# Performance work log

Measured on AMD Instinct MI355X. Metric: run time of the kernel, lower is better.

## Reference

```python
import math
import jax, jax.numpy as jnp
import numpy as np

IMG = 512; P = 16; CIN = 3; COUT = 3; E = 768; NHEADS = 12; L = 8
NPH = IMG // P            # 32 patches per side
N = NPH * NPH             # 1024 tokens (must match learned 1024x1024 attn bias)
HD = E // NHEADS          # 64
INTER = min(E // 2, 128)  # 128, OutputProjection intermediate
EPS = 1e-5


def _sin_pe(n_h, n_w, d):
    # faithful port of get_2d_sinusoidal_encoding (second half stays zero)
    pe = np.zeros((n_h, n_w, d), dtype=np.float32)
    dq, dh = d // 4, d // 2
    div = np.exp(np.arange(0, dq, 2, dtype=np.float32) * (-math.log(10000.0) / dq))
    pr = np.arange(n_h, dtype=np.float32)[:, None]
    pc = np.arange(n_w, dtype=np.float32)[:, None]
    pe[:, :, 0:dq:2] = np.sin(pr * div)[:, None, :]
    pe[:, :, 1:dq:2] = np.cos(pr * div)[:, None, :]
    pe[:, :, dq:dh:2] = np.sin(pc * div)[None, :, :]
    pe[:, :, dq + 1:dh:2] = np.cos(pc * div)[None, :, :]
    return jnp.asarray(pe.reshape(-1, d))


def _ln(x, g, b):
    m = x.mean(-1, keepdims=True)
    v = ((x - m) ** 2).mean(-1, keepdims=True)
    return (x - m) * jax.lax.rsqrt(v + EPS) * g + b


def setup_inputs():
    key = jax.random.key(0)
    ks = iter(jax.random.split(key, 32))
    def nrm(shape, scale=0.02):
        return jax.random.normal(next(ks), shape, jnp.float32) * scale
    return {
        'x': jax.random.normal(next(ks), (2, CIN, IMG, IMG), jnp.float32),
        'conv_w': nrm((E, CIN, P, P)), 'conv_b': jnp.zeros((E,), jnp.float32),
        'ln1_g': jnp.ones((L, E), jnp.float32), 'ln1_b': jnp.zeros((L, E), jnp.float32),
        'qkv_w': nrm((L, 3 * E, E)),
        'proj_w': nrm((L, E, E)), 'proj_b': jnp.zeros((L, E), jnp.float32),
        'attn_bias': jax.random.normal(next(ks), (L, N, N), jnp.float32),  # torch.randn init
        'ln2_g': jnp.ones((L, E), jnp.float32), 'ln2_b': jnp.zeros((L, E), jnp.float32),
        'mlp_w1': nrm((L, 2 * E, E)), 'mlp_b1': jnp.zeros((L, 2 * E), jnp.float32),
        'mlp_w2': nrm((L, E, 2 * E)), 'mlp_b2': jnp.zeros((L, E), jnp.float32),
        'op_w1': nrm((INTER, E)), 'op_b1': jnp.zeros((INTER,), jnp.float32),
        'op_w2': nrm((P * P * COUT, INTER)), 'op_b2': jnp.zeros((P * P * COUT,), jnp.float32),
        'ag_wg': nrm((1, COUT), 0.2), 'ag_bng_w': jnp.ones((), jnp.float32), 'ag_bng_b': jnp.zeros((), jnp.float32),
        'ag_wx': nrm((1, CIN), 0.2), 'ag_bnx_w': jnp.ones((), jnp.float32), 'ag_bnx_b': jnp.zeros((), jnp.float32),
        'ag_psi_w': jnp.full((), 0.5, jnp.float32), 'ag_psi_b': jnp.zeros((), jnp.float32),
    }


def reference(x, conv_w, conv_b, ln1_g, ln1_b, qkv_w, proj_w, proj_b, attn_bias,
              ln2_g, ln2_b, mlp_w1, mlp_b1, mlp_w2, mlp_b2,
              op_w1, op_b1, op_w2, op_b2,
              ag_wg, ag_bng_w, ag_bng_b, ag_wx, ag_bnx_w, ag_bnx_b, ag_psi_w, ag_psi_b):
    B = x.shape[0]
    # --- VisionTransformerInput: patch-embed conv (stride == kernel) as reshape+GEMM ---
    xp = x.reshape(B, CIN, NPH, P, NPH, P).transpose(0, 2, 4, 1, 3, 5).reshape(B, N, CIN * P * P)
    t = xp @ conv_w.reshape(E, -1).T + conv_b
    t = t + _sin_pe(NPH, NPH, E)[None]

    # --- encoder blocks (scan over stacked per-layer params) ---
    def block(t, p):
        y = _ln(t, p['ln1_g'], p['ln1_b'])
        qkv = (y @ p['qkv_w'].T).reshape(B, N, 3, NHEADS, HD).transpose(2, 0, 3, 1, 4)
        q, k, v = qkv[0], qkv[1], qkv[2]
        s = jnp.einsum('bhnd,bhmd->bhnm', q, k) / math.sqrt(HD)
        # NOTE: relative_position_bias is computed but never added in the source (dead code);
        # only the learned (N,N) bias parameter is added.
        s = s + p['attn_bias'][None, None]
        a = jax.nn.softmax(s, axis=-1)
        o = jnp.einsum('bhnm,bhmd->bhnd', a, v).transpose(0, 2, 1, 3).reshape(B, N, E)
        o = o @ p['proj_w'].T + p['proj_b']
        t = t + (y + o)  # MHA has an extra internal residual (out = x + out) in the source
        h = _ln(t, p['ln2_g'], p['ln2_b'])
        h = jax.nn.gelu(h @ p['mlp_w1'].T + p['mlp_b1'], approximate=False) @ p['mlp_w2'].T + p['mlp_b2']
        return t + h, None

    stacked = {'ln1_g': ln1_g, 'ln1_b': ln1_b, 'qkv_w': qkv_w, 'proj_w': proj_w,
               'proj_b': proj_b, 'attn_bias': attn_bias, 'ln2_g': ln2_g, 'ln2_b': ln2_b,
               'mlp_w1': mlp_w1, 'mlp_b1': mlp_b1, 'mlp_w2': mlp_w2, 'mlp_b2': mlp_b2}
    t, _ = jax.lax.scan(block, t, stacked)

    # --- OutputProjection: MLP -> Fold -> attention gate -> (identity) interpolate ---
    h = jax.nn.relu(t @ op_w1.T + op_b1) @ op_w2.T + op_b2  # (B, N, C*P*P)
    # nn.Fold(kernel=stride=P): columns interpreted as (C, P, P)
    g = h.reshape(B, NPH, NPH, COUT, P, P).transpose(0, 3, 1, 4, 2, 5).reshape(B, COUT, IMG, IMG)
    inv = 1.0 / math.sqrt(1.0 + EPS)  # BatchNorm eval: running_mean=0, running_var=1
    g1 = jnp.einsum('bchw,oc->bohw', g, ag_wg) * (inv * ag_bng_w) + ag_bng_b
    x1 = jnp.einsum('bchw,oc->bohw', x, ag_wx) * (inv * ag_bnx_w) + ag_bnx_b
    psi = jax.nn.sigmoid(jax.nn.relu(g1 + x1) * ag_psi_w + ag_psi_b)
    out = g * (x * psi)  # x * att_gate's psi == skip_gated; then x_fold * skip_gated
    # F.interpolate to (output_size, output_size) with output_size == image_size: identity
    return out
```

## Files before the change

kernel.cpp:

```cpp
#include <hip/hip_runtime.h>
#include <math.h>

typedef unsigned short u16;
typedef unsigned int u32;
typedef __attribute__((ext_vector_type(8))) short bf16x8;
typedef __attribute__((ext_vector_type(16))) float f32x16;
typedef __attribute__((ext_vector_type(4))) float f4v;
typedef __attribute__((ext_vector_type(4))) u32 u32x4;

#define MFMA(a, b, c) __builtin_amdgcn_mfma_f32_32x32x16_bf16(a, b, c, 0, 0, 0)

#define SYNC_STEP() do {                                   \
    asm volatile("s_waitcnt vmcnt(0)" ::: "memory");       \
    __builtin_amdgcn_s_barrier();                          \
    __builtin_amdgcn_sched_barrier(0);                     \
} while (0)

#define SYNC_CNT_LIT(nlit) do {                                    \
    asm volatile("s_waitcnt vmcnt(" #nlit ")" ::: "memory");       \
    __builtin_amdgcn_s_barrier();                                  \
    __builtin_amdgcn_sched_barrier(0);                             \
} while (0)

__device__ __forceinline__ float bf2f(u16 h) { return __uint_as_float(((u32)h) << 16); }

__device__ __forceinline__ void split2(float v, u16& h, u16& l) {
    u32 u = __float_as_uint(v);
    u32 hr = (u + 0x7FFFu + ((u >> 16) & 1u)) & 0xFFFF0000u;
    h = (u16)(hr >> 16);
    float lf = v - __uint_as_float(hr);
    u32 ul = __float_as_uint(lf);
    l = (u16)((ul + 0x7FFFu + ((ul >> 16) & 1u)) >> 16);
}

__device__ __forceinline__ u32 cvtpk(float lo, float hi) {
    u32 r;
    asm("v_cvt_pk_bf16_f32 %0, %1, %2" : "=v"(r) : "v"(lo), "v"(hi));
    return r;
}

__device__ __forceinline__ void swap32(u32& a, u32& b, int hi) {
    u32 ta = (u32)__shfl_xor((int)a, 32);
    u32 tb = (u32)__shfl_xor((int)b, 32);
    u32 na = hi ? tb : a;
    u32 nb = hi ? b : ta;
    a = na; b = nb;
}

__device__ __forceinline__ void repack(const f32x16& v, int base, int hi, bf16x8& fh, bf16x8& fl) {
    float p0 = v[base + 0], p1 = v[base + 1], p2 = v[base + 2], p3 = v[base + 3];
    float p4 = v[base + 4], p5 = v[base + 5], p6 = v[base + 6], p7 = v[base + 7];
    u32 X0 = cvtpk(p0, p1), X1 = cvtpk(p2, p3), X4 = cvtpk(p4, p5), X5 = cvtpk(p6, p7);
    float r0 = p0 - __uint_as_float(X0 << 16);
    float r1 = p1 - __uint_as_float(X0 & 0xFFFF0000u);
    float r2 = p2 - __uint_as_float(X1 << 16);
    float r3 = p3 - __uint_as_float(X1 & 0xFFFF0000u);
    float r4 = p4 - __uint_as_float(X4 << 16);
    float r5 = p5 - __uint_as_float(X4 & 0xFFFF0000u);
    float r6 = p6 - __uint_as_float(X5 << 16);
    float r7 = p7 - __uint_as_float(X5 & 0xFFFF0000u);
    u32 L0 = cvtpk(r0, r1), L1 = cvtpk(r2, r3), L4 = cvtpk(r4, r5), L5 = cvtpk(r6, r7);
    swap32(X0, X4, hi); swap32(X1, X5, hi);
    swap32(L0, L4, hi); swap32(L1, L5, hi);
    u32x4 th = {X0, X1, X4, X5};
    u32x4 tl = {L0, L1, L4, L5};
    fh = __builtin_bit_cast(bf16x8, th);
    fl = __builtin_bit_cast(bf16x8, tl);
}

__global__ __launch_bounds__(256) void pe_kernel(float* __restrict__ pe) {
    int idx = blockIdx.x * 256 + threadIdx.x;
    int n = idx / 768, d = idx - n * 768;
    float v = 0.0f;
    if (d < 384) {
        int pos = (d < 192) ? (n >> 5) : (n & 31);
        int dd  = (d < 192) ? d : d - 192;
        int j2  = dd & ~1;
        float dv  = expf((float)j2 * (-9.210340371976184f / 192.0f));
        float ang = (float)pos * dv;
        v = (dd & 1) ? cosf(ang) : sinf(ang);
    }
    pe[idx] = v;
}

__global__ __launch_bounds__(256) void gather_kernel(const float* __restrict__ x,
                                                     u16* __restrict__ xph,
                                                     u16* __restrict__ xpl) {
    int idx = blockIdx.x * 256 + threadIdx.x;
    int m = idx / 768, col = idx - m * 768;
    int b = m >> 10, n = m & 1023;
    int ci = col >> 8, rem = col & 255;
    int pr = rem >> 4, pc = rem & 15;
    int hh = ((n >> 5) << 4) + pr;
    int ww = ((n & 31) << 4) + pc;
    float v = x[(((size_t)(b * 3 + ci) * 512) + hh) * 512 + ww];
    split2(v, xph[idx], xpl[idx]);
}

__global__ __launch_bounds__(256) void fsplit(const float* __restrict__ in,
                                              u16* __restrict__ h, u16* __restrict__ l, int n4) {
    int i = blockIdx.x * 256 + threadIdx.x;
    if (i >= n4) return;
    float4 v = ((const float4*)in)[i];
    int o = i * 4;
    split2(v.x, h[o], l[o]);
    split2(v.y, h[o + 1], l[o + 1]);
    split2(v.z, h[o + 2], l[o + 2]);
    split2(v.w, h[o + 3], l[o + 3]);
}

__global__ __launch_bounds__(256) void wsplit_layer(const float* __restrict__ qkvw,
                                                    const float* __restrict__ projw,
                                                    const float* __restrict__ w1,
                                                    const float* __restrict__ w2,
                                                    u16* __restrict__ wh, u16* __restrict__ wl) {
    int i4 = blockIdx.x * 256 + threadIdx.x;
    if (i4 >= 1179648) return;
    size_t idx = (size_t)i4 * 4;
    const float* src; size_t off;
    if (idx < 1769472)      { src = qkvw;  off = idx; }
    else if (idx < 2359296) { src = projw; off = idx - 1769472; }
    else if (idx < 3538944) { src = w1;    off = idx - 2359296; }
    else                    { src = w2;    off = idx - 3538944; }
    float4 v = *(const float4*)(src + off);
    split2(v.x, wh[idx], wl[idx]);
    split2(v.y, wh[idx + 1], wl[idx + 1]);
    split2(v.z, wh[idx + 2], wl[idx + 2]);
    split2(v.w, wh[idx + 3], wl[idx + 3]);
}

__global__ __launch_bounds__(256) void btrans(const float* __restrict__ src, float* __restrict__ dst) {
    __shared__ float tl[32][33];
    int bx = blockIdx.x & 31, by = blockIdx.x >> 5;
    int tx = threadIdx.x & 31, ty = threadIdx.x >> 5;
#pragma unroll
    for (int j = 0; j < 4; ++j)
        tl[ty + j * 8][tx] = src[(size_t)(by * 32 + ty + j * 8) * 1024 + bx * 32 + tx];
    __syncthreads();
#pragma unroll
    for (int j = 0; j < 4; ++j)
        dst[(size_t)(bx * 32 + ty + j * 8) * 1024 + by * 32 + tx] = tl[tx][ty + j * 8];
}

__global__ __launch_bounds__(256) void ln_kernel(const float* __restrict__ x,
                                                 const float* __restrict__ g,
                                                 const float* __restrict__ b,
                                                 u16* __restrict__ yh, u16* __restrict__ yl) {
    int row = blockIdx.x, tid = threadIdx.x;
    int wid = tid >> 6, lane = tid & 63;
    const float* xr = x + (size_t)row * 768;
    float v0 = xr[tid], v1 = xr[tid + 256], v2 = xr[tid + 512];
    __shared__ float ws[8];
    float sum = v0 + v1 + v2;
#pragma unroll
    for (int off = 32; off > 0; off >>= 1) sum += __shfl_xor(sum, off);
    if (lane == 0) ws[wid] = sum;
    __syncthreads();
    float mean = (ws[0] + ws[1] + ws[2] + ws[3]) * (1.0f / 768.0f);
    float d0 = v0 - mean, d1 = v1 - mean, d2 = v2 - mean;
    float vs = d0 * d0 + d1 * d1 + d2 * d2;
#pragma unroll
    for (int off = 32; off > 0; off >>= 1) vs += __shfl_xor(vs, off);
    if (lane == 0) ws[4 + wid] = vs;
    __syncthreads();
    float rstd = rsqrtf((ws[4] + ws[5] + ws[6] + ws[7]) * (1.0f / 768.0f) + 1e-5f);
    size_t o = (size_t)row * 768;
    split2(d0 * rstd * g[tid]       + b[tid],       yh[o + tid],       yl[o + tid]);
    split2(d1 * rstd * g[tid + 256] + b[tid + 256], yh[o + tid + 256], yl[o + tid + 256]);
    split2(d2 * rstd * g[tid + 512] + b[tid + 512], yh[o + tid + 512], yl[o + tid + 512]);
}

__device__ __forceinline__ int mrow(int r) { return (r + (r >> 2)) & 3; }

template <int MODE>
__global__ __launch_bounds__(256, 2) void gemm_sp(const u16* __restrict__ Ah, const u16* __restrict__ Al,
                                                  const u16* __restrict__ Bh, const u16* __restrict__ Bl,
                                                  const float* __restrict__ bias,
                                                  const float* __restrict__ res,
                                                  const float* __restrict__ auxf,
                                                  const u16* __restrict__ auxh, const u16* __restrict__ auxl,
                                                  float* __restrict__ C, u16* __restrict__ Ch, u16* __restrict__ Cl,
                                                  int M, int N, int K, int nby) {
    __shared__ u16 SH[36864];
    u16* As = SH;
    u16* Bs = SH + 12288;
    int tid = threadIdx.x;
    int wid = tid >> 6, lane = tid & 63;
    int hi = lane >> 5;
    int lq = lane & 31;

    int nwg = gridDim.x;
    int q8 = nwg >> 3;
    int swz = (blockIdx.x & 7) * q8 + (blockIdx.x >> 3);
    int cb = swz / nby, rb = swz - cb * nby;
    int m0 = rb * 64, n0 = cb * 128;

    f32x16 acc0 = {}, acc1 = {};

    auto stage = [&](int buf, int kt) {
#pragma unroll
        for (int c = 0; c < 2; ++c) {
            const u16* G = c ? Al : Ah;
            int row = wid * 16 + (lane >> 2);
            int ch = (lane & 3) ^ mrow(row);
            const u16* g = G + (size_t)(m0 + row) * K + kt + ch * 8;
            __builtin_amdgcn_global_load_lds((const __attribute__((address_space(1))) u32*)g,
                                             (__attribute__((address_space(3))) u32*)&As[(buf * 2 + c) * 2048 + (wid * 16) * 32],
                                             16, 0, 0);
        }
#pragma unroll
        for (int c = 0; c < 2; ++c) {
            const u16* G = c ? Bl : Bh;
#pragma unroll
            for (int j = 0; j < 2; ++j) {
                int row = wid * 32 + j * 16 + (lane >> 2);
                int ch = (lane & 3) ^ mrow(row);
                const u16* g = G + (size_t)(n0 + row) * K + kt + ch * 8;
                __builtin_amdgcn_global_load_lds((const __attribute__((address_space(1))) u32*)g,
                                                 (__attribute__((address_space(3))) u32*)&Bs[(buf * 2 + c) * 4096 + (wid * 32 + j * 16) * 32],
                                                 16, 0, 0);
            }
        }
    };

    int ar  = (wid >> 1) * 32 + lq;
    int br0 = (wid & 1) * 64 + lq;
    int br1 = br0 + 32;

    auto compute = [&](int buf) {
#pragma unroll
        for (int kc = 0; kc < 2; ++kc) {
            int gc = (kc << 1) | hi;
            int oA  = ar  * 32 + ((gc ^ mrow(ar))  << 3);
            int oB0 = br0 * 32 + ((gc ^ mrow(br0)) << 3);
            int oB1 = br1 * 32 + ((gc ^ mrow(br1)) << 3);
            bf16x8 ah  = *(const bf16x8*)(As + (buf * 2 + 0) * 2048 + oA);
            bf16x8 al  = *(const bf16x8*)(As + (buf * 2 + 1) * 2048 + oA);
            bf16x8 b0h = *(const bf16x8*)(Bs + (buf * 2 + 0) * 4096 + oB0);
            bf16x8 b0l = *(const bf16x8*)(Bs + (buf * 2 + 1) * 4096 + oB0);
            bf16x8 b1h = *(const bf16x8*)(Bs + (buf * 2 + 0) * 4096 + oB1);
            bf16x8 b1l = *(const bf16x8*)(Bs + (buf * 2 + 1) * 4096 + oB1);
            acc0 = MFMA(ah, b0h, acc0);
            acc0 = MFMA(ah, b0l, acc0);
            acc0 = MFMA(al, b0h, acc0);
            acc1 = MFMA(ah, b1h, acc1);
            acc1 = MFMA(ah, b1l, acc1);
            acc1 = MFMA(al, b1h, acc1);
        }
    };

    int nk = K >> 5;
    stage(0, 0);
    stage(1, 32);
    int t = 0;
    for (; t < nk - 1; ++t) {
        SYNC_CNT_LIT(6);
        if (t + 2 < nk) stage((t + 2) % 3, (t + 2) << 5);
        compute(t % 3);
    }
    SYNC_STEP();
    compute(t % 3);

    auto epi = [&](const f32x16& a, int ncol) {
        int col = n0 + ncol + lq;
        int rb2 = m0 + (wid >> 1) * 32 + (hi << 2);
#pragma unroll
        for (int r = 0; r < 16; ++r) {
            int row = rb2 + (r & 3) + ((r >> 2) << 3);
            float v = a[r];
            size_t o = (size_t)row * N + col;
            if (MODE == 1) C[o] = v + bias[col] + auxf[(size_t)(row & 1023) * N + col];
            else if (MODE == 2) C[o] = res[o] + (bf2f(auxh[o]) + bf2f(auxl[o])) + v + bias[col];
            else if (MODE == 4) C[o] = res[o] + v + bias[col];
            else if (MODE == 5) {
                v += bias[col];
                v = fmaxf(v, 0.0f);
                split2(v, Ch[o], Cl[o]);
            }
            else if (MODE == 6) C[o] = v + bias[col];
        }
    };
    epi(acc0, (wid & 1) * 64);
    epi(acc1, (wid & 1) * 64 + 32);
}

template <int MODE>
__global__ __launch_bounds__(256, 2) void gemm_sq(const u16* __restrict__ Ah, const u16* __restrict__ Al,
                                                  const u16* __restrict__ Bh, const u16* __restrict__ Bl,
                                                  const float* __restrict__ bias,
                                                  u16* __restrict__ Ch, u16* __restrict__ Cl,
                                                  u16* __restrict__ Cth, u16* __restrict__ Ctl,
                                                  int M, int N, int K, int nby) {
    __shared__ u16 SH[32768];
    int tid = threadIdx.x;
    int wid = tid >> 6, lane = tid & 63;
    int hi = lane >> 5;
    int lq = lane & 31;
    int wm = wid >> 1, wn = wid & 1;

    int nwg = gridDim.x;
    int q8 = nwg >> 3;
    int swz = (blockIdx.x & 7) * q8 + (blockIdx.x >> 3);
    int cb = swz / nby, rb = swz - cb * nby;
    int m0 = rb * 128, n0 = cb * 128;

    f32x16 acc00 = {}, acc01 = {}, acc10 = {}, acc11 = {};

    const u16* srcs[4] = {Ah, Al, Bh, Bl};
    auto stage = [&](int buf, int kt) {
        const u16* G = srcs[wid];
        int rbase = (wid < 2) ? m0 : n0;
#pragma unroll
        for (int i = 0; i < 8; ++i) {
            int row = i * 16 + (lane >> 2);
            int ch = (lane & 3) ^ mrow(row);
            const u16* g = G + (size_t)(rbase + row) * K + kt + ch * 8;
            __builtin_amdgcn_global_load_lds((const __attribute__((address_space(1))) u32*)g,
                                             (__attribute__((address_space(3))) u32*)&SH[buf * 16384 + wid * 4096 + i * 512],
                                             16, 0, 0);
        }
    };

    int ar0 = wm * 64 + lq, ar1 = ar0 + 32;
    int br0 = wn * 64 + lq, br1 = br0 + 32;

    auto compute = [&](int buf) {
        const u16* SAh = SH + buf * 16384;
        const u16* SAl = SAh + 4096;
        const u16* SBh = SAl + 4096;
        const u16* SBl = SBh + 4096;
#pragma unroll
        for (int kc = 0; kc < 2; ++kc) {
            int gc = (kc << 1) | hi;
            int oA0 = ar0 * 32 + ((gc ^ mrow(ar0)) << 3);
            int oA1 = ar1 * 32 + ((gc ^ mrow(ar1)) << 3);
            int oB0 = br0 * 32 + ((gc ^ mrow(br0)) << 3);
            int oB1 = br1 * 32 + ((gc ^ mrow(br1)) << 3);
            bf16x8 a0h = *(const bf16x8*)(SAh + oA0);
            bf16x8 a0l = *(const bf16x8*)(SAl + oA0);
            bf16x8 a1h = *(const bf16x8*)(SAh + oA1);
            bf16x8 a1l = *(const bf16x8*)(SAl + oA1);
            bf16x8 b0h = *(const bf16x8*)(SBh + oB0);
            bf16x8 b0l = *(const bf16x8*)(SBl + oB0);
            bf16x8 b1h = *(const bf16x8*)(SBh + oB1);
            bf16x8 b1l = *(const bf16x8*)(SBl + oB1);
            acc00 = MFMA(a0h, b0h, acc00);
            acc00 = MFMA(a0h, b0l, acc00);
            acc00 = MFMA(a0l, b0h, acc00);
            acc01 = MFMA(a0h, b1h, acc01);
            acc01 = MFMA(a0h, b1l, acc01);
            acc01 = MFMA(a0l, b1h, acc01);
            acc10 = MFMA(a1h, b0h, acc10);
            acc10 = MFMA(a1h, b0l, acc10);
            acc10 = MFMA(a1l, b0h, acc10);
            acc11 = MFMA(a1h, b1h, acc11);
            acc11 = MFMA(a1h, b1l, acc11);
            acc11 = MFMA(a1l, b1h, acc11);
        }
    };

    int nk = K >> 5;
    stage(0, 0);
    for (int t = 0; t < nk; ++t) {
        SYNC_STEP();
        if (t + 1 < nk) stage((t + 1) & 1, (t + 1) << 5);
        compute(t & 1);
    }

    if (MODE == 7 && n0 >= 1536) {
        int bb = m0 >> 10;
        int nbase = m0 & 1023;
#pragma unroll
        for (int P = 0; P < 2; ++P) {
            __syncthreads();
            if (wm == P) {
                auto scat = [&](const f32x16& a, int fm, int fn) {
                    int c = wn * 64 + fn * 32 + lq;
                    int rbl = fm * 32 + (hi << 2);
#pragma unroll
                    for (int r = 0; r < 16; ++r) {
                        int rr = rbl + (r & 3) + ((r >> 2) << 3);
                        u16 hv, lv;
                        split2(a[r], hv, lv);
                        SH[c * 68 + rr] = hv;
                        SH[8704 + c * 68 + rr] = lv;
                    }
                };
                scat(acc00, 0, 0); scat(acc01, 0, 1); scat(acc10, 1, 0); scat(acc11, 1, 1);
            }
            __syncthreads();
#pragma unroll
            for (int pass = 0; pass < 4; ++pass) {
                int c2 = pass * 32 + (tid >> 3);
                int ch8 = tid & 7;
                int hcol = (n0 - 1536) + c2;
                int h2 = hcol >> 6, hd = hcol & 63;
                size_t dst = ((size_t)(bb * 12 + h2) * 64 + hd) * 1024 + nbase + P * 64 + ch8 * 8;
                int so = c2 * 68 + ch8 * 8;
                u32x4 ph = {*(const u32*)&SH[so], *(const u32*)&SH[so + 2],
                            *(const u32*)&SH[so + 4], *(const u32*)&SH[so + 6]};
                u32x4 pl = {*(const u32*)&SH[8704 + so], *(const u32*)&SH[8704 + so + 2],
                            *(const u32*)&SH[8704 + so + 4], *(const u32*)&SH[8704 + so + 6]};
                *(u32x4*)(Cth + dst) = ph;
                *(u32x4*)(Ctl + dst) = pl;
            }
        }
        return;
    }

    auto epi = [&](const f32x16& a, int fm, int fn) {
        int col = n0 + wn * 64 + fn * 32 + lq;
        int rb2 = m0 + wm * 64 + fm * 32 + (hi << 2);
#pragma unroll
        for (int r = 0; r < 16; ++r) {
            int row = rb2 + (r & 3) + ((r >> 2) << 3);
            float v = a[r];
            if (MODE == 3) {
                size_t o = (size_t)row * N + col;
                v += bias[col];
                v = 0.5f * v * (1.0f + erff(v * 0.70710678118654752f));
                split2(v, Ch[o], Cl[o]);
            } else if (MODE == 7) {
                size_t o7 = (size_t)row * 1536 + col;
                split2(v, Ch[o7], Cl[o7]);
            }
        }
    };
    epi(acc00, 0, 0); epi(acc01, 0, 1); epi(acc10, 1, 0); epi(acc11, 1, 1);
}

__global__ __launch_bounds__(256, 2) void attn_mfma(const u16* __restrict__ qh, const u16* __restrict__ ql,
                                                    const u16* __restrict__ vth, const u16* __restrict__ vtl,
                                                    const float* __restrict__ biasT,
                                                    u16* __restrict__ oh, u16* __restrict__ ol) {
    __shared__ u16 smem[2][4][2048];
    int tid = threadIdx.x;
    int wid = tid >> 6, lane = tid & 63;
    int s = wid & 1, p = wid >> 1;
    int lq = lane & 31;
    int hi = lane >> 5;
    int id = blockIdx.x;
    int xcd = id & 7;
    int j = id >> 3;
    int bh = xcd * 3 + (j >> 4);
    int qt = j & 15;
    int b = bh / 12, h = bh % 12;
    int bq0 = qt * 64;
    int gq = bq0 + s * 32 + lq;

    bf16x8 qfh[4], qfl[4];
    {
        size_t qo = (size_t)(b * 1024 + gq) * 1536 + h * 64 + hi * 8;
#pragma unroll
        for (int ks = 0; ks < 4; ++ks) {
            qfh[ks] = *(const bf16x8*)(qh + qo + ks * 16);
            qfl[ks] = *(const bf16x8*)(ql + qo + ks * 16);
        }
    }

    f32x16 oa = {}, ob = {};
    float m_i = -1e30f, l_i = 0.0f;

    auto stage = [&](int kb) {
        if (s == 0) {
#pragma unroll
            for (int c = 0; c < 2; ++c) {
                const u16* G = c ? ql : qh;
#pragma unroll
                for (int i = 0; i < 4; ++i) {
                    int r = 8 * i + (lane >> 3);
                    int cl = (lane & 7) ^ (r & 7);
                    const u16* g = G + (size_t)(b * 1024 + kb + r) * 1536 + 768 + h * 64 + cl * 8;
                    __builtin_amdgcn_global_load_lds((const __attribute__((address_space(1))) u32*)g,
                                                     (__attribute__((address_space(3))) u32*)&smem[p][c][i * 512],
                                                     16, 0, 0);
                }
            }
        } else {
#pragma unroll
            for (int c = 0; c < 2; ++c) {
                const u16* G = c ? vtl : vth;
#pragma unroll
                for (int i = 0; i < 4; ++i) {
                    int r = 16 * i + (lane >> 2);
                    int cl = (lane & 3) ^ ((r >> 1) & 3);
                    const u16* g = G + ((size_t)(b * 12 + h) * 64 + r) * 1024 + kb + cl * 8;
                    __builtin_amdgcn_global_load_lds((const __attribute__((address_space(1))) u32*)g,
                                                     (__attribute__((address_space(3))) u32*)&smem[p][2 + c][i * 512],
                                                     16, 0, 0);
                }
            }
        }
    };

    auto loadBias = [&](float (&bb)[16], int kb) {
        const float* bbase = biasT + (size_t)(kb + 4 * hi) * 1024 + gq;
#pragma unroll
        for (int g2 = 0; g2 < 4; ++g2)
#pragma unroll
            for (int q = 0; q < 4; ++q)
                bb[g2 * 4 + q] = bbase[(size_t)(g2 * 8 + q) * 1024];
    };

    auto compute = [&](const float (&bb)[16]) {
        const u16* Kh = &smem[p][0][0];
        const u16* Kl = &smem[p][1][0];
        const u16* Vh = &smem[p][2][0];
        const u16* Vl = &smem[p][3][0];
        f32x16 s0 = {}, s1 = {};
        __builtin_amdgcn_s_setprio(1);
#pragma unroll
        for (int ks = 0; ks < 2; ++ks) {
            int offA = lq * 64 + (((2 * ks + hi) ^ (lq & 7)) << 3);
            int offB = lq * 64 + (((2 * (ks + 2) + hi) ^ (lq & 7)) << 3);
            bf16x8 khA = *(const bf16x8*)(Kh + offA);
            bf16x8 klA = *(const bf16x8*)(Kl + offA);
            bf16x8 khB = *(const bf16x8*)(Kh + offB);
            bf16x8 klB = *(const bf16x8*)(Kl + offB);
            s0 = MFMA(khA, qfh[ks], s0);
            s1 = MFMA(khB, qfh[ks + 2], s1);
            s0 = MFMA(khA, qfl[ks], s0);
            s1 = MFMA(khB, qfl[ks + 2], s1);
            s0 = MFMA(klA, qfh[ks], s0);
            s1 = MFMA(klB, qfh[ks + 2], s1);
        }
        __builtin_amdgcn_s_setprio(0);
        bf16x8 vf[2][4];
#pragma unroll
        for (int kslot = 0; kslot < 2; ++kslot) {
            int offa = lq * 32 + (((2 * kslot + hi) ^ ((lq >> 1) & 3)) << 3);
            vf[kslot][0] = *(const bf16x8*)(Vh + offa);
            vf[kslot][1] = *(const bf16x8*)(Vh + offa + 1024);
            vf[kslot][2] = *(const bf16x8*)(Vl + offa);
            vf[kslot][3] = *(const bf16x8*)(Vl + offa + 1024);
        }
        f32x16 sa;
#pragma unroll
        for (int r = 0; r < 16; ++r) sa[r] = (s0[r] + s1[r]) * 0.125f + bb[r];
        float m01 = fmaxf(sa[0], sa[1]),  m23 = fmaxf(sa[2], sa[3]);
        float m45 = fmaxf(sa[4], sa[5]),  m67 = fmaxf(sa[6], sa[7]);
        float m89 = fmaxf(sa[8], sa[9]),  mab = fmaxf(sa[10], sa[11]);
        float mcd = fmaxf(sa[12], sa[13]), mef = fmaxf(sa[14], sa[15]);
        float pm = fmaxf(fmaxf(fmaxf(m01, m23), fmaxf(m45, m67)),
                         fmaxf(fmaxf(m89, mab), fmaxf(mcd, mef)));
        pm = fmaxf(pm, __shfl_xor(pm, 32));
        if (__any(pm > m_i + 8.0f)) {
            float mnew = fmaxf(m_i, pm);
            float scl = __expf(m_i - mnew);
            m_i = mnew;
            l_i *= scl;
#pragma unroll
            for (int r = 0; r < 16; ++r) {
                int qr = (r & 3) + 8 * (r >> 2) + 4 * hi;
                float fr = __shfl(scl, qr);
                oa[r] *= fr; ob[r] *= fr;
            }
        }
        float ls = 0.0f;
#pragma unroll
        for (int r = 0; r < 16; ++r) { sa[r] = __expf(sa[r] - m_i); ls += sa[r]; }
        ls += __shfl_xor(ls, 32);
        l_i += ls;
        __builtin_amdgcn_s_setprio(1);
#pragma unroll
        for (int kslot = 0; kslot < 2; ++kslot) {
            bf16x8 ph, pl;
            repack(sa, kslot * 8, hi, ph, pl);
            oa = MFMA(ph, vf[kslot][0], oa);
            oa = MFMA(ph, vf[kslot][2], oa);
            oa = MFMA(pl, vf[kslot][0], oa);
            ob = MFMA(ph, vf[kslot][1], ob);
            ob = MFMA(ph, vf[kslot][3], ob);
            ob = MFMA(pl, vf[kslot][1], ob);
        }
        __builtin_amdgcn_s_setprio(0);
    };

    float bbA[16], bbB[16];
    stage(p * 32);
    loadBias(bbA, p * 32);
    for (int ss = 0; ss < 16; ss += 2) {
        SYNC_STEP();
        if (ss + 1 < 16) loadBias(bbB, (2 * (ss + 1) + p) * 32);
        compute(bbA);
        __syncthreads();
        if (ss + 1 < 16) stage((2 * (ss + 1) + p) * 32);
        SYNC_STEP();
        if (ss + 2 < 16) loadBias(bbA, (2 * (ss + 2) + p) * 32);
        if (ss + 1 < 16) compute(bbB);
        __syncthreads();
        if (ss + 2 < 16) stage((2 * (ss + 2) + p) * 32);
    }

    float* mlb = (float*)((char*)smem + 16384);
    mlb[((s * 2 + p) * 2 + 0) * 32 + lq] = m_i;
    mlb[((s * 2 + p) * 2 + 1) * 32 + lq] = l_i;
    __syncthreads();
    float mo  = mlb[((s * 2 + (p ^ 1)) * 2 + 0) * 32 + lq];
    float lo_ = mlb[((s * 2 + (p ^ 1)) * 2 + 1) * 32 + lq];
    float M = fmaxf(m_i, mo);
    float ea = __expf(m_i - M), eb = __expf(mo - M);
    float L = ea * l_i + eb * lo_;
    float f = ea / L;
    float frv[16];
#pragma unroll
    for (int r = 0; r < 16; ++r) frv[r] = __shfl(f, (r & 3) + 8 * (r >> 2) + 4 * hi);
    float* ox = (float*)((char*)smem + s * 8192);
    if (p == 1) {
#pragma unroll
        for (int r = 0; r < 16; ++r) {
            int qr = (r & 3) + 8 * (r >> 2) + 4 * hi;
            ox[qr * 64 + lq] = oa[r] * frv[r];
            ox[qr * 64 + 32 + lq] = ob[r] * frv[r];
        }
    }
    __syncthreads();
    if (p == 0) {
#pragma unroll
        for (int r = 0; r < 16; ++r) {
            int qr = (r & 3) + 8 * (r >> 2) + 4 * hi;
            float va = oa[r] * frv[r] + ox[qr * 64 + lq];
            float vb = ob[r] * frv[r] + ox[qr * 64 + 32 + lq];
            size_t d = (size_t)(b * 1024 + bq0 + s * 32 + qr) * 768 + h * 64;
            split2(va, oh[d + lq], ol[d + lq]);
            split2(vb, oh[d + 32 + lq], ol[d + 32 + lq]);
        }
    }
}

__global__ __launch_bounds__(256) void fold_gate(const float* __restrict__ hbuf,
                                                 const float* __restrict__ xin,
                                                 const float* __restrict__ wg,
                                                 const float* __restrict__ bngw,
                                                 const float* __restrict__ bngb,
                                                 const float* __restrict__ wx,
                                                 const float* __restrict__ bnxw,
                                                 const float* __restrict__ bnxb,
                                                 const float* __restrict__ psiw,
                                                 const float* __restrict__ psib,
                                                 float* __restrict__ out) {
    int idx = blockIdx.x * 256 + threadIdx.x;
    int b = idx >> 18;
    int rem = idx & 262143;
    int hh = rem >> 9, ww = rem & 511;
    int n = ((hh >> 4) << 5) + (ww >> 4);
    int pr = hh & 15, pc = ww & 15;
    const float* hrow = hbuf + (size_t)(b * 1024 + n) * 768 + pr * 16 + pc;
    float g0 = hrow[0], g1 = hrow[256], g2 = hrow[512];
    size_t xoff = ((size_t)(b * 3) * 512 + hh) * 512 + ww;
    float x0 = xin[xoff], x1 = xin[xoff + 262144], x2 = xin[xoff + 524288];
    float inv = rsqrtf(1.0f + 1e-5f);
    float gg = (g0 * wg[0] + g1 * wg[1] + g2 * wg[2]) * inv * bngw[0] + bngb[0];
    float xx = (x0 * wx[0] + x1 * wx[1] + x2 * wx[2]) * inv * bnxw[0] + bnxb[0];
    float z = gg + xx;
    z = z > 0.0f ? z : 0.0f;
    float psi = 1.0f / (1.0f + expf(-(z * psiw[0] + psib[0])));
    out[xoff]          = g0 * x0 * psi;
    out[xoff + 262144] = g1 * x1 * psi;
    out[xoff + 524288] = g2 * x2 * psi;
}

extern "C" void kernel_launch(void* const* d_in, const int* in_sizes, int n_in,
                              void* d_out, int out_size, void* d_ws, size_t ws_size,
                              hipStream_t stream) {
    (void)in_sizes; (void)n_in; (void)out_size; (void)ws_size;
    const float* x       = (const float*)d_in[0];
    const float* conv_w  = (const float*)d_in[1];
    const float* conv_b  = (const float*)d_in[2];
    const float* ln1_g   = (const float*)d_in[3];
    const float* ln1_b   = (const float*)d_in[4];
    const float* qkv_w   = (const float*)d_in[5];
    const float* proj_w  = (const float*)d_in[6];
    const float* proj_b  = (const float*)d_in[7];
    const float* attn_bs = (const float*)d_in[8];
    const float* ln2_g   = (const float*)d_in[9];
    const float* ln2_b   = (const float*)d_in[10];
    const float* mlp_w1  = (const float*)d_in[11];
    const float* mlp_b1  = (const float*)d_in[12];
    const float* mlp_w2  = (const float*)d_in[13];
    const float* mlp_b2  = (const float*)d_in[14];
    const float* op_w1   = (const float*)d_in[15];
    const float* op_b1   = (const float*)d_in[16];
    const float* op_w2   = (const float*)d_in[17];
    const float* op_b2   = (const float*)d_in[18];
    const float* ag_wg   = (const float*)d_in[19];
    const float* ag_bngw = (const float*)d_in[20];
    const float* ag_bngb = (const float*)d_in[21];
    const float* ag_wx   = (const float*)d_in[22];
    const float* ag_bnxw = (const float*)d_in[23];
    const float* ag_bnxb = (const float*)d_in[24];
    const float* ag_psiw = (const float*)d_in[25];
    const float* ag_psib = (const float*)d_in[26];
    float* out = (float*)d_out;

    char* w8 = (char*)d_ws;
    float* t     = (float*)(w8);
    u16* yh      = (u16*)(w8 + 6291456);
    u16* yl      = (u16*)(w8 + 9437184);
    u16* ath     = (u16*)(w8 + 12582912);
    u16* atl     = (u16*)(w8 + 15728640);
    u16* mh      = (u16*)(w8 + 18874368);
    u16* ml      = (u16*)(w8 + 25165824);
    u16* qh      = (u16*)(w8 + 31457280);
    u16* ql      = (u16*)(w8 + 37748736);
    u16* wh      = (u16*)(w8 + 44040192);
    u16* wl      = (u16*)(w8 + 53477376);
    float* biasT = (float*)(w8 + 62914560);
    float* pe  = (float*)qh;
    u16* xph = mh; u16* xpl = ml;
    u16* vth = mh; u16* vtl = ml;
    float* oph2 = (float*)qh;
    u16* o1h = ath; u16* o1l = atl;

    const size_t W_QKV = 0, W_PROJ = 1769472, W_MLP1 = 2359296, W_MLP2 = 3538944;

    pe_kernel<<<3072, 256, 0, stream>>>(pe);
    gather_kernel<<<6144, 256, 0, stream>>>(x, xph, xpl);
    fsplit<<<576, 256, 0, stream>>>(conv_w, wh, wl, 147456);
    gemm_sp<1><<<192, 256, 0, stream>>>(xph, xpl, wh, wl, conv_b, nullptr, pe,
                                        nullptr, nullptr, t, nullptr, nullptr, 2048, 768, 768, 32);

    for (int l = 0; l < 8; ++l) {
        wsplit_layer<<<4608, 256, 0, stream>>>(qkv_w + (size_t)l * 1769472, proj_w + (size_t)l * 589824,
                                               mlp_w1 + (size_t)l * 1179648, mlp_w2 + (size_t)l * 1179648,
                                               wh, wl);
        btrans<<<1024, 256, 0, stream>>>(attn_bs + (size_t)l * 1048576, biasT);
        ln_kernel<<<2048, 256, 0, stream>>>(t, ln1_g + l * 768, ln1_b + l * 768, yh, yl);
        gemm_sq<7><<<288, 256, 0, stream>>>(yh, yl, wh + W_QKV, wl + W_QKV, nullptr,
                                            qh, ql, vth, vtl, 2048, 2304, 768, 16);
        attn_mfma<<<384, 256, 0, stream>>>(qh, ql, vth, vtl, biasT, ath, atl);
        gemm_sp<2><<<192, 256, 0, stream>>>(ath, atl, wh + W_PROJ, wl + W_PROJ, proj_b + l * 768,
                                            t, nullptr, yh, yl, t, nullptr, nullptr, 2048, 768, 768, 32);
        ln_kernel<<<2048, 256, 0, stream>>>(t, ln2_g + l * 768, ln2_b + l * 768, yh, yl);
        gemm_sq<3><<<192, 256, 0, stream>>>(yh, yl, wh + W_MLP1, wl + W_MLP1, mlp_b1 + l * 1536,
                                            mh, ml, nullptr, nullptr, 2048, 1536, 768, 16);
        gemm_sp<4><<<192, 256, 0, stream>>>(mh, ml, wh + W_MLP2, wl + W_MLP2, mlp_b2 + l * 768,
                                            t, nullptr, nullptr, nullptr, t, nullptr, nullptr,
                                            2048, 768, 1536, 32);
    }

    fsplit<<<1536, 256, 0, stream>>>(t, yh, yl, 393216);
    fsplit<<<96, 256, 0, stream>>>(op_w1, wh, wl, 24576);
    fsplit<<<96, 256, 0, stream>>>(op_w2, wh + 131072, wl + 131072, 24576);
    gemm_sp<5><<<32, 256, 0, stream>>>(yh, yl, wh, wl, op_b1, nullptr, nullptr,
                                       nullptr, nullptr, nullptr, o1h, o1l, 2048, 128, 768, 32);
    gemm_sp<6><<<192, 256, 0, stream>>>(o1h, o1l, wh + 131072, wl + 131072, op_b2, nullptr,
                                        nullptr, nullptr, nullptr, oph2, nullptr, nullptr,
                                        2048, 768, 128, 32);
    fold_gate<<<2048, 256, 0, stream>>>(oph2, x, ag_wg, ag_bngw, ag_bngb,
                                        ag_wx, ag_bnxw, ag_bnxb, ag_psiw, ag_psib, out);
}
```

Measured before the change: 1.426 ms.

## Split attention over key halves with separate merge kernel

Splits each attention block's 1024-key sweep into two halves processed by separate workgroups (flash-decoding style). This doubles the grid from 384 to 768 blocks. Each half writes unnormalized fp32 partial outputs plus its row max and sum. A new merge kernel then rescales, normalizes and splits the result into bf16 hi/lo for the projection GEMM. The aim is better occupancy across the GPU's compute units, at the cost of an extra launch and extra fp32 partial traffic through workspace buffers reused from other stages.

```diff
diff --git a/kernel.cpp b/kernel.cpp
--- a/kernel.cpp
+++ b/kernel.cpp
@@ -432,7 +432,9 @@
 __global__ __launch_bounds__(256, 2) void attn_mfma(const u16* __restrict__ qh, const u16* __restrict__ ql,
                                                     const u16* __restrict__ vth, const u16* __restrict__ vtl,
                                                     const float* __restrict__ biasT,
-                                                    u16* __restrict__ oh, u16* __restrict__ ol) {
+                                                    float* __restrict__ O0,
+                                                    float* __restrict__ O1a, float* __restrict__ O1b,
+                                                    float* __restrict__ ML) {
     __shared__ u16 smem[2][4][2048];
     int tid = threadIdx.x;
     int wid = tid >> 6, lane = tid & 63;
@@ -442,8 +444,10 @@
     int id = blockIdx.x;
     int xcd = id & 7;
     int j = id >> 3;
-    int bh = xcd * 3 + (j >> 4);
-    int qt = j & 15;
+    int bh = xcd * 3 + (j >> 5);
+    int r5 = j & 31;
+    int qt = r5 >> 1;
+    int kh = r5 & 1;
     int b = bh / 12, h = bh % 12;
     int bq0 = qt * 64;
     int gq = bq0 + s * 32 + lq;
@@ -460,6 +464,8 @@
 
     f32x16 oa = {}, ob = {};
     float m_i = -1e30f, l_i = 0.0f;
+
+    auto kb_of = [&](int ss) { return kh * 512 + (2 * ss + p) * 32; };
 
     auto stage = [&](int kb) {
         if (s == 0) {
@@ -577,19 +583,19 @@
     };
 
     float bbA[16], bbB[16];
-    stage(p * 32);
-    loadBias(bbA, p * 32);
-    for (int ss = 0; ss < 16; ss += 2) {
+    stage(kb_of(0));
+    loadBias(bbA, kb_of(0));
+    for (int ss = 0; ss < 8; ss += 2) {
         SYNC_STEP();
-        if (ss + 1 < 16) loadBias(bbB, (2 * (ss + 1) + p) * 32);
+        if (ss + 1 < 8) loadBias(bbB, kb_of(ss + 1));
         compute(bbA);
         __syncthreads();
-        if (ss + 1 < 16) stage((2 * (ss + 1) + p) * 32);
+        if (ss + 1 < 8) stage(kb_of(ss + 1));
         SYNC_STEP();
-        if (ss + 2 < 16) loadBias(bbA, (2 * (ss + 2) + p) * 32);
-        if (ss + 1 < 16) compute(bbB);
+        if (ss + 2 < 8) loadBias(bbA, kb_of(ss + 2));
+        if (ss + 1 < 8) compute(bbB);
         __syncthreads();
-        if (ss + 2 < 16) stage((2 * (ss + 2) + p) * 32);
+        if (ss + 2 < 8) stage(kb_of(ss + 2));
     }
 
     float* mlb = (float*)((char*)smem + 16384);
@@ -599,12 +605,10 @@
     float mo  = mlb[((s * 2 + (p ^ 1)) * 2 + 0) * 32 + lq];
     float lo_ = mlb[((s * 2 + (p ^ 1)) * 2 + 1) * 32 + lq];
     float M = fmaxf(m_i, mo);
-    float ea = __expf(m_i - M), eb = __expf(mo - M);
-    float L = ea * l_i + eb * lo_;
-    float f = ea / L;
+    float ea = __expf(m_i - M);
     float frv[16];
 #pragma unroll
-    for (int r = 0; r < 16; ++r) frv[r] = __shfl(f, (r & 3) + 8 * (r >> 2) + 4 * hi);
+    for (int r = 0; r < 16; ++r) frv[r] = __shfl(ea, (r & 3) + 8 * (r >> 2) + 4 * hi);
     float* ox = (float*)((char*)smem + s * 8192);
     if (p == 1) {
 #pragma unroll
@@ -616,15 +620,52 @@
     }
     __syncthreads();
     if (p == 0) {
+        float* Op = (kh == 0) ? (O0 + (size_t)bh * 65536)
+                              : ((bh < 13) ? (O1a + (size_t)bh * 65536)
+                                           : (O1b + (size_t)(bh - 13) * 65536));
 #pragma unroll
         for (int r = 0; r < 16; ++r) {
             int qr = (r & 3) + 8 * (r >> 2) + 4 * hi;
             float va = oa[r] * frv[r] + ox[qr * 64 + lq];
             float vb = ob[r] * frv[r] + ox[qr * 64 + 32 + lq];
-            size_t d = (size_t)(b * 1024 + bq0 + s * 32 + qr) * 768 + h * 64;
-            split2(va, oh[d + lq], ol[d + lq]);
-            split2(vb, oh[d + 32 + lq], ol[d + 32 + lq]);
-        }
+            size_t d = (size_t)(bq0 + s * 32 + qr) * 64;
+            Op[d + lq] = va;
+            Op[d + 32 + lq] = vb;
+        }
+        if (hi == 0) {
+            float Lm = ea * l_i + __expf(mo - M) * lo_;
+            int qg = bh * 1024 + bq0 + s * 32 + lq;
+            ML[kh * 49152 + qg] = M;
+            ML[kh * 49152 + 24576 + qg] = Lm;
+        }
+    }
+}
+
+__global__ __launch_bounds__(256) void attn_merge(const float* __restrict__ O0,
+                                                  const float* __restrict__ O1a,
+                                                  const float* __restrict__ O1b,
+                                                  const float* __restrict__ ML,
+                                                  u16* __restrict__ oh, u16* __restrict__ ol) {
+    int gid = blockIdx.x * 256 + threadIdx.x;
+    int row = gid >> 4;
+    int d0 = (gid & 15) * 4;
+    int bh = row >> 10, q = row & 1023;
+    int b = bh / 12, h = bh - b * 12;
+    float m0 = ML[row];
+    float l0 = ML[24576 + row];
+    float m1 = ML[49152 + row];
+    float l1 = ML[49152 + 24576 + row];
+    float M = fmaxf(m0, m1);
+    float e0 = __expf(m0 - M), e1 = __expf(m1 - M);
+    float invL = 1.0f / (l0 * e0 + l1 * e1);
+    const float* p0 = O0 + (size_t)row * 64 + d0;
+    const float* p1 = ((bh < 13) ? (O1a + (size_t)bh * 65536) : (O1b + (size_t)(bh - 13) * 65536))
+                      + (size_t)q * 64 + d0;
+    size_t dst = (size_t)(b * 1024 + q) * 768 + h * 64 + d0;
+#pragma unroll
+    for (int k = 0; k < 4; ++k) {
+        float v = (p0[k] * e0 + p1[k] * e1) * invL;
+        split2(v, oh[dst + k], ol[dst + k]);
     }
 }
 
@@ -711,6 +752,12 @@
     u16* vth = mh; u16* vtl = ml;
     float* oph2 = (float*)qh;
     u16* o1h = ath; u16* o1l = atl;
+    float* O0  = (float*)(w8 + 12582912);
+    float* O1a = (float*)(w8 + 44040192);
+    float* O1b = (float*)(w8 + 53477376);
+    float* MLp = (float*)(w8 + 22020096);
+    u16* aoh = qh;
+    u16* aol = ql;
 
     const size_t W_QKV = 0, W_PROJ = 1769472, W_MLP1 = 2359296, W_MLP2 = 3538944;
 
@@ -728,8 +775,9 @@
         ln_kernel<<<2048, 256, 0, stream>>>(t, ln1_g + l * 768, ln1_b + l * 768, yh, yl);
         gemm_sq<7><<<288, 256, 0, stream>>>(yh, yl, wh + W_QKV, wl + W_QKV, nullptr,
                                             qh, ql, vth, vtl, 2048, 2304, 768, 16);
-        attn_mfma<<<384, 256, 0, stream>>>(qh, ql, vth, vtl, biasT, ath, atl);
-        gemm_sp<2><<<192, 256, 0, stream>>>(ath, atl, wh + W_PROJ, wl + W_PROJ, proj_b + l * 768,
+        attn_mfma<<<768, 256, 0, stream>>>(qh, ql, vth, vtl, biasT, O0, O1a, O1b, MLp);
+        attn_merge<<<1536, 256, 0, stream>>>(O0, O1a, O1b, MLp, aoh, aol);
+        gemm_sp<2><<<192, 256, 0, stream>>>(aoh, aol, wh + W_PROJ, wl + W_PROJ, proj_b + l * 768,
                                             t, nullptr, yh, yl, t, nullptr, nullptr, 2048, 768, 768, 32);
         ln_kernel<<<2048, 256, 0, stream>>>(t, ln2_g + l * 768, ln2_b + l * 768, yh, yl);
         gemm_sq<3><<<192, 256, 0, stream>>>(yh, yl, wh + W_MLP1, wl + W_MLP1, mlp_b1 + l * 1536,
```

After: 1.459 ms. +2.3%, slower.

## Double attention key tile to 64 per stage and drop bias prefetch pipelining

Applied to the files above, without the earlier changes.

Each warp-pair now processes 64 keys per step instead of 32, doubling the LDS staging buffers and halving the number of loop iterations and barriers. The V tile is re-laid out to a 64-key row with the same XOR swizzle as K. The bias is now loaded inside compute rather than prefetched one step ahead, and the setprio hints are removed. This trades fewer synchronisations for more registers and LDS per block, which may reduce occupancy and expose bias-load latency.

```diff
diff --git a/kernel.cpp b/kernel.cpp
--- a/kernel.cpp
+++ b/kernel.cpp
@@ -433,7 +433,7 @@
                                                     const u16* __restrict__ vth, const u16* __restrict__ vtl,
                                                     const float* __restrict__ biasT,
                                                     u16* __restrict__ oh, u16* __restrict__ ol) {
-    __shared__ u16 smem[2][4][2048];
+    __shared__ u16 smem[2][4][4096];
     int tid = threadIdx.x;
     int wid = tid >> 6, lane = tid & 63;
     int s = wid & 1, p = wid >> 1;
@@ -447,6 +447,7 @@
     int b = bh / 12, h = bh % 12;
     int bq0 = qt * 64;
     int gq = bq0 + s * 32 + lq;
+    size_t vbase = (size_t)bh * 65536;
 
     bf16x8 qfh[4], qfl[4];
     {
@@ -467,7 +468,7 @@
             for (int c = 0; c < 2; ++c) {
                 const u16* G = c ? ql : qh;
 #pragma unroll
-                for (int i = 0; i < 4; ++i) {
+                for (int i = 0; i < 8; ++i) {
                     int r = 8 * i + (lane >> 3);
                     int cl = (lane & 7) ^ (r & 7);
                     const u16* g = G + (size_t)(b * 1024 + kb + r) * 1536 + 768 + h * 64 + cl * 8;
@@ -481,10 +482,10 @@
             for (int c = 0; c < 2; ++c) {
                 const u16* G = c ? vtl : vth;
 #pragma unroll
-                for (int i = 0; i < 4; ++i) {
-                    int r = 16 * i + (lane >> 2);
-                    int cl = (lane & 3) ^ ((r >> 1) & 3);
-                    const u16* g = G + ((size_t)(b * 12 + h) * 64 + r) * 1024 + kb + cl * 8;
+                for (int i = 0; i < 8; ++i) {
+                    int r = 8 * i + (lane >> 3);
+                    int cl = (lane & 7) ^ (r & 7);
+                    const u16* g = G + vbase + (size_t)r * 1024 + kb + cl * 8;
                     __builtin_amdgcn_global_load_lds((const __attribute__((address_space(1))) u32*)g,
                                                      (__attribute__((address_space(3))) u32*)&smem[p][2 + c][i * 512],
                                                      16, 0, 0);
@@ -493,56 +494,54 @@
         }
     };
 
-    auto loadBias = [&](float (&bb)[16], int kb) {
-        const float* bbase = biasT + (size_t)(kb + 4 * hi) * 1024 + gq;
-#pragma unroll
-        for (int g2 = 0; g2 < 4; ++g2)
-#pragma unroll
-            for (int q = 0; q < 4; ++q)
-                bb[g2 * 4 + q] = bbase[(size_t)(g2 * 8 + q) * 1024];
-    };
-
-    auto compute = [&](const float (&bb)[16]) {
+    auto compute = [&](int kb) {
         const u16* Kh = &smem[p][0][0];
         const u16* Kl = &smem[p][1][0];
         const u16* Vh = &smem[p][2][0];
         const u16* Vl = &smem[p][3][0];
-        f32x16 s0 = {}, s1 = {};
-        __builtin_amdgcn_s_setprio(1);
-#pragma unroll
-        for (int ks = 0; ks < 2; ++ks) {
+        const float* bbase = biasT + (size_t)(kb + 4 * hi) * 1024 + gq;
+        float bb[32];
+#pragma unroll
+        for (int g2 = 0; g2 < 4; ++g2)
+#pragma unroll
+            for (int q = 0; q < 4; ++q) {
+                bb[g2 * 4 + q]      = bbase[(size_t)(g2 * 8 + q) * 1024];
+                bb[16 + g2 * 4 + q] = bbase[(size_t)(32 + g2 * 8 + q) * 1024];
+            }
+        f32x16 sa = {}, sb = {};
+#pragma unroll
+        for (int ks = 0; ks < 4; ++ks) {
             int offA = lq * 64 + (((2 * ks + hi) ^ (lq & 7)) << 3);
-            int offB = lq * 64 + (((2 * (ks + 2) + hi) ^ (lq & 7)) << 3);
+            int offB = offA + 2048;
             bf16x8 khA = *(const bf16x8*)(Kh + offA);
             bf16x8 klA = *(const bf16x8*)(Kl + offA);
             bf16x8 khB = *(const bf16x8*)(Kh + offB);
             bf16x8 klB = *(const bf16x8*)(Kl + offB);
-            s0 = MFMA(khA, qfh[ks], s0);
-            s1 = MFMA(khB, qfh[ks + 2], s1);
-            s0 = MFMA(khA, qfl[ks], s0);
-            s1 = MFMA(khB, qfl[ks + 2], s1);
-            s0 = MFMA(klA, qfh[ks], s0);
-            s1 = MFMA(klB, qfh[ks + 2], s1);
-        }
-        __builtin_amdgcn_s_setprio(0);
-        bf16x8 vf[2][4];
-#pragma unroll
-        for (int kslot = 0; kslot < 2; ++kslot) {
-            int offa = lq * 32 + (((2 * kslot + hi) ^ ((lq >> 1) & 3)) << 3);
-            vf[kslot][0] = *(const bf16x8*)(Vh + offa);
-            vf[kslot][1] = *(const bf16x8*)(Vh + offa + 1024);
-            vf[kslot][2] = *(const bf16x8*)(Vl + offa);
-            vf[kslot][3] = *(const bf16x8*)(Vl + offa + 1024);
-        }
-        f32x16 sa;
-#pragma unroll
-        for (int r = 0; r < 16; ++r) sa[r] = (s0[r] + s1[r]) * 0.125f + bb[r];
-        float m01 = fmaxf(sa[0], sa[1]),  m23 = fmaxf(sa[2], sa[3]);
-        float m45 = fmaxf(sa[4], sa[5]),  m67 = fmaxf(sa[6], sa[7]);
-        float m89 = fmaxf(sa[8], sa[9]),  mab = fmaxf(sa[10], sa[11]);
-        float mcd = fmaxf(sa[12], sa[13]), mef = fmaxf(sa[14], sa[15]);
-        float pm = fmaxf(fmaxf(fmaxf(m01, m23), fmaxf(m45, m67)),
-                         fmaxf(fmaxf(m89, mab), fmaxf(mcd, mef)));
+            sa = MFMA(khA, qfh[ks], sa);
+            sb = MFMA(khB, qfh[ks], sb);
+            sa = MFMA(khA, qfl[ks], sa);
+            sb = MFMA(khB, qfl[ks], sb);
+            sa = MFMA(klA, qfh[ks], sa);
+            sb = MFMA(klB, qfh[ks], sb);
+        }
+        bf16x8 vf[4][4];
+#pragma unroll
+        for (int kslot = 0; kslot < 4; ++kslot) {
+            int off0 = lq * 64 + (((2 * kslot + hi) ^ (lq & 7)) << 3);
+            int off1 = off0 + 2048;
+            vf[kslot][0] = *(const bf16x8*)(Vh + off0);
+            vf[kslot][1] = *(const bf16x8*)(Vh + off1);
+            vf[kslot][2] = *(const bf16x8*)(Vl + off0);
+            vf[kslot][3] = *(const bf16x8*)(Vl + off1);
+        }
+#pragma unroll
+        for (int r = 0; r < 16; ++r) {
+            sa[r] = sa[r] * 0.125f + bb[r];
+            sb[r] = sb[r] * 0.125f + bb[16 + r];
+        }
+        float pm = fmaxf(sa[0], sb[0]);
+#pragma unroll
+        for (int r = 1; r < 16; ++r) pm = fmaxf(pm, fmaxf(sa[r], sb[r]));
         pm = fmaxf(pm, __shfl_xor(pm, 32));
         if (__any(pm > m_i + 8.0f)) {
             float mnew = fmaxf(m_i, pm);
@@ -558,14 +557,17 @@
         }
         float ls = 0.0f;
 #pragma unroll
-        for (int r = 0; r < 16; ++r) { sa[r] = __expf(sa[r] - m_i); ls += sa[r]; }
+        for (int r = 0; r < 16; ++r) {
+            sa[r] = __expf(sa[r] - m_i); ls += sa[r];
+            sb[r] = __expf(sb[r] - m_i); ls += sb[r];
+        }
         ls += __shfl_xor(ls, 32);
         l_i += ls;
-        __builtin_amdgcn_s_setprio(1);
-#pragma unroll
-        for (int kslot = 0; kslot < 2; ++kslot) {
+#pragma unroll
+        for (int kslot = 0; kslot < 4; ++kslot) {
             bf16x8 ph, pl;
-            repack(sa, kslot * 8, hi, ph, pl);
+            if (kslot < 2) repack(sa, (kslot & 1) * 8, hi, ph, pl);
+            else           repack(sb, (kslot & 1) * 8, hi, ph, pl);
             oa = MFMA(ph, vf[kslot][0], oa);
             oa = MFMA(ph, vf[kslot][2], oa);
             oa = MFMA(pl, vf[kslot][0], oa);
@@ -573,26 +575,17 @@
             ob = MFMA(ph, vf[kslot][3], ob);
             ob = MFMA(pl, vf[kslot][1], ob);
         }
-        __builtin_amdgcn_s_setprio(0);
     };
 
-    float bbA[16], bbB[16];
-    stage(p * 32);
-    loadBias(bbA, p * 32);
-    for (int ss = 0; ss < 16; ss += 2) {
+    stage(p * 64);
+    for (int ss = 0; ss < 8; ++ss) {
         SYNC_STEP();
-        if (ss + 1 < 16) loadBias(bbB, (2 * (ss + 1) + p) * 32);
-        compute(bbA);
+        compute((2 * ss + p) * 64);
         __syncthreads();
-        if (ss + 1 < 16) stage((2 * (ss + 1) + p) * 32);
-        SYNC_STEP();
-        if (ss + 2 < 16) loadBias(bbA, (2 * (ss + 2) + p) * 32);
-        if (ss + 1 < 16) compute(bbB);
-        __syncthreads();
-        if (ss + 2 < 16) stage((2 * (ss + 2) + p) * 32);
-    }
-
-    float* mlb = (float*)((char*)smem + 16384);
+        if (ss + 1 < 8) stage((2 * (ss + 1) + p) * 64);
+    }
+
+    float* mlb = (float*)((char*)smem + 32768);
     mlb[((s * 2 + p) * 2 + 0) * 32 + lq] = m_i;
     mlb[((s * 2 + p) * 2 + 1) * 32 + lq] = l_i;
     __syncthreads();
```

Measured after the change: 1.394 ms (median of 2 runs). 1.02x faster.
